# Performance work log

Measured on AMD Instinct MI355X. Metric: run time of the kernel, lower is better.

The kernel has to match this reference:

```python
import jax, jax.numpy as jnp
import numpy as np
from jax import lax

USER_NUM = 60000
ITEM_NUM = 40000
N_NODES = USER_NUM + ITEM_NUM
EMB = 64
NNZ = 3200000
N_LAYERS = 3
ALPHA = 0.1


def setup_inputs() -> dict:
    key = jax.random.key(0)
    k1, k2, k3, k4, k5 = jax.random.split(key, 5)
    rows = jax.random.randint(k1, (NNZ,), 0, N_NODES, dtype=jnp.int32)
    cols = jax.random.randint(k2, (NNZ,), 0, N_NODES, dtype=jnp.int32)
    # normalized adjacency values are small positives
    vals = jax.random.uniform(k3, (NNZ,), dtype=jnp.float32) * 0.05
    user_emb = jax.random.normal(k4, (USER_NUM, EMB), dtype=jnp.float32) * 0.1
    item_emb = jax.random.normal(k5, (ITEM_NUM, EMB), dtype=jnp.float32) * 0.1
    return {"rows": rows, "cols": cols, "vals": vals,
            "user_emb": user_emb, "item_emb": item_emb}


def reference(rows, cols, vals, user_emb, item_emb):
    # ego = cat(user, item); e_out starts at zeros (first forward call).
    ego = jnp.concatenate([user_emb, item_emb], axis=0)  # [N, d]
    e0 = jnp.zeros_like(ego)

    def step(e, _):
        # torch.sparse.mm(A, e.clone().detach()) -> SpMM with stop_gradient,
        # matching the original's detach of the propagated state.
        gathered = vals[:, None] * lax.stop_gradient(e)[cols]  # [nnz, d]
        msg = jax.ops.segment_sum(gathered, rows, num_segments=N_NODES)
        e_new = (1.0 - ALPHA) * msg + ego
        return e_new, None

    e_out, _ = lax.scan(step, e0, None, length=N_LAYERS)
    return e_out[:USER_NUM], e_out[USER_NUM:]
```

## Files before the change

kernel.cpp:

```cpp
#include <hip/hip_runtime.h>
#include <hip/hip_fp16.h>


#define USER_NUM 60000
#define ITEM_NUM 40000
#define N_NODES  100000
#define EMB      64
#define NNZ      3200000
#define OMA       0.9f
#define BR       128
#define NB       782
#define TILE     4096
#define CAPB     4480
#define EPT      9

typedef float f32x4 __attribute__((ext_vector_type(4)));

__global__ __launch_bounds__(512) void bucket_scatter(const int* __restrict__ rows,
                                                      const int* __restrict__ cols,
                                                      const float* __restrict__ vals,
                                                      const float* __restrict__ ue,
                                                      const float* __restrict__ ie,
                                                      __half* __restrict__ ego_h,
                                                      int* __restrict__ bcursor,
                                                      int2* __restrict__ ebuf) {
    __shared__ int bins[NB + 1];
    __shared__ int lcur[NB];
    __shared__ int wsum[8];
    __shared__ int2 stage[TILE];
    __shared__ unsigned short sbk[TILE];
    int t = threadIdx.x;
    int lane = t & 63, w = t >> 6;

    {
        const int total8 = N_NODES * EMB / 8;
        const size_t usz = (size_t)USER_NUM * EMB;
        int u0 = blockIdx.x * 1024;
#pragma unroll
        for (int q = 0; q < 2; ++q) {
            int u = u0 + t + 512 * q;
            if (u < total8) {
                size_t f0 = (size_t)u * 8;
                const float4* s4 = (f0 < usz) ? (const float4*)(ue + f0)
                                              : (const float4*)(ie + (f0 - usz));
                float4 x = s4[0], y = s4[1];
                union { float4 f4; __half2 h2[4]; } o;
                o.h2[0] = __floats2half2_rn(x.x, x.y);
                o.h2[1] = __floats2half2_rn(x.z, x.w);
                o.h2[2] = __floats2half2_rn(y.x, y.y);
                o.h2[3] = __floats2half2_rn(y.z, y.w);
                ((float4*)ego_h)[u] = o.f4;
            }
        }
    }

    for (int b = t; b <= NB; b += 512) bins[b] = 0;
    __syncthreads();

    int e0 = blockIdx.x * TILE;
    int mybk[8], mypk[8];
    float myv[8];
#pragma unroll
    for (int j = 0; j < 8; ++j) {
        int i = e0 + t + 512 * j;
        mybk[j] = -1;
        if (i < NNZ) {
            int r = rows[i], c = cols[i];
            myv[j]  = vals[i] * OMA;
            mybk[j] = r >> 7;
            mypk[j] = c | ((r & 127) << 17);
            atomicAdd(&bins[mybk[j]], 1);
        }
    }
    __syncthreads();

    int b0 = t * 2;
    int r0 = (b0     < NB) ? bins[b0]     : 0;
    int r1 = (b0 + 1 < NB) ? bins[b0 + 1] : 0;
    int s = r0 + r1;
    int incl = s;
#pragma unroll
    for (int off = 1; off < 64; off <<= 1) {
        int v = __shfl_up(incl, off, 64);
        if (lane >= off) incl += v;
    }
    if (lane == 63) wsum[w] = incl;
    __syncthreads();
    int prefix = 0;
#pragma unroll
    for (int i = 0; i < 8; ++i) if (i < w) prefix += wsum[i];
    int excl = prefix + incl - s;
    if (b0     < NB) { bins[b0]     = excl; lcur[b0]     = excl; excl += r0; }
    if (b0 + 1 < NB) { bins[b0 + 1] = excl; lcur[b0 + 1] = excl; }
    if (t == 511) bins[NB] = prefix + incl;
    __syncthreads();

#pragma unroll
    for (int j = 0; j < 8; ++j) {
        if (mybk[j] >= 0) {
            int p = atomicAdd(&lcur[mybk[j]], 1);
            stage[p] = make_int2(mypk[j], __float_as_int(myv[j]));
            sbk[p] = (unsigned short)mybk[j];
        }
    }
    __syncthreads();

    for (int b = t; b < NB; b += 512) {
        int st = bins[b], en = bins[b + 1];
        int c = en - st;
        if (c > 0) lcur[b] = b * CAPB + atomicAdd(&bcursor[b], c) - st;
    }
    __syncthreads();

    int total = bins[NB];
    for (int i = t; i < total; i += 512) {
        int bk = sbk[i];
        ebuf[(size_t)(lcur[bk] + i)] = stage[i];
    }
}

__global__ __launch_bounds__(512) void sort_spmm1(const int* __restrict__ bcursor,
                                                  int2* __restrict__ ebuf,
                                                  int* __restrict__ row_start,
                                                  int* __restrict__ row_end,
                                                  const __half* __restrict__ ego_h,
                                                  const float* __restrict__ ue,
                                                  const float* __restrict__ ie,
                                                  __half* __restrict__ e2h) {
    __shared__ int2 stage[CAPB];
    __shared__ int rhist[BR], rofs[BR], rcur[BR];
    int bk = blockIdx.x, t = threadIdx.x;
    int s = bk * CAPB;
    int cnt = min(bcursor[bk], CAPB);

    if (t < BR) rhist[t] = 0;
    __syncthreads();

    int2 ev[EPT]; int erow[EPT];
#pragma unroll
    for (int j = 0; j < EPT; ++j) {
        int i = t + 512 * j;
        erow[j] = -1;
        if (i < cnt) {
            ev[j] = ebuf[(size_t)(s + i)];
            erow[j] = (ev[j].x >> 17) & 127;
            atomicAdd(&rhist[erow[j]], 1);
        }
    }
    __syncthreads();
    if (t < 64) {
        int h0 = rhist[2 * t], h1 = rhist[2 * t + 1];
        int pair = h0 + h1;
        int incl = pair;
#pragma unroll
        for (int off = 1; off < 64; off <<= 1) {
            int v = __shfl_up(incl, off, 64);
            if (t >= off) incl += v;
        }
        int base = incl - pair;
        rofs[2 * t]     = base;      rcur[2 * t]     = base;
        rofs[2 * t + 1] = base + h0; rcur[2 * t + 1] = base + h0;
    }
    __syncthreads();
    if (t < BR) {
        int r = (bk << 7) + t;
        if (r < N_NODES) {
            row_start[r] = s + rofs[t];
            row_end[r]   = s + rofs[t] + rhist[t];
        }
    }
#pragma unroll
    for (int j = 0; j < EPT; ++j) {
        if (erow[j] >= 0) {
            int p = atomicAdd(&rcur[erow[j]], 1);
            stage[p] = ev[j];
        }
    }
    __syncthreads();
    for (int i = t; i < cnt; i += 512) ebuf[(size_t)(s + i)] = stage[i];

    int lane  = t & 15;
    int qbase = (t & 63) & ~15;
    int g = t >> 4;
    const float2* srcv = (const float2*)ego_h;
#pragma unroll
    for (int rr = 0; rr < 4; ++rr) {
        int rl = (g << 2) | rr;
        int r  = (bk << 7) + rl;
        if (r >= N_NODES) break;
        const float* egop = (r < USER_NUM) ? (ue + (size_t)r * EMB)
                                           : (ie + (size_t)(r - USER_NUM) * EMB);
        float4 acc = ((const float4*)egop)[lane];
        int ss = rofs[rl];
        int ee = ss + rhist[rl];
        for (int k = ss; k < ee; k += 16) {
            int idx = k + lane;
            int2 cv = (idx < ee) ? stage[idx] : make_int2(0, 0);
#pragma unroll
            for (int j = 0; j < 16; ++j) {
                int   cj = __shfl(cv.x, qbase + j, 64) & 0x1FFFF;
                float vj = __int_as_float(__shfl(cv.y, qbase + j, 64));
                union { float2 f2; __half2 h2[2]; } u;
                u.f2 = srcv[(size_t)cj * 16 + lane];
                float2 a = __half22float2(u.h2[0]);
                float2 b = __half22float2(u.h2[1]);
                acc.x += vj * a.x; acc.y += vj * a.y;
                acc.z += vj * b.x; acc.w += vj * b.y;
            }
        }
        union { float2 f2; __half2 h2[2]; } o;
        o.h2[0] = __floats2half2_rn(acc.x, acc.y);
        o.h2[1] = __floats2half2_rn(acc.z, acc.w);
        ((float2*)e2h)[(size_t)r * 16 + lane] = o.f2;
    }
}

__global__ __launch_bounds__(256) void spmm2(const int* __restrict__ row_start,
                                             const int* __restrict__ row_end,
                                             const int2* __restrict__ colval,
                                             const __half* __restrict__ src,
                                             const float* __restrict__ ue,
                                             const float* __restrict__ ie,
                                             float* __restrict__ outb) {
    int tid = blockIdx.x * 256 + threadIdx.x;
    int r = tid >> 4;
    if (r >= N_NODES) return;
    int lane  = threadIdx.x & 15;
    int qbase = (threadIdx.x & 63) & ~15;

    const float* egop = (r < USER_NUM) ? (ue + (size_t)r * EMB)
                                       : (ie + (size_t)(r - USER_NUM) * EMB);
    float4 acc = ((const float4*)egop)[lane];
    const float2* srcv = (const float2*)src;
    const unsigned long long* cv8 = (const unsigned long long*)colval;
    int s = row_start[r], e = row_end[r];

    unsigned long long cv = 0;
    if (s + lane < e) cv = __builtin_nontemporal_load(&cv8[(size_t)(s + lane)]);
    for (int k = s; k < e; k += 16) {
        int idxn = k + 16 + lane;
        unsigned long long nv = 0;
        if (idxn < e) nv = __builtin_nontemporal_load(&cv8[(size_t)idxn]);
        int cx = (int)(cv & 0xFFFFFFFFull), cy = (int)(cv >> 32);
#pragma unroll
        for (int j = 0; j < 16; ++j) {
            int   cj = __shfl(cx, qbase + j, 64) & 0x1FFFF;
            float vj = __int_as_float(__shfl(cy, qbase + j, 64));
            union { float2 f2; __half2 h2[2]; } u;
            u.f2 = srcv[(size_t)cj * 16 + lane];
            float2 a = __half22float2(u.h2[0]);
            float2 b = __half22float2(u.h2[1]);
            acc.x += vj * a.x; acc.y += vj * a.y;
            acc.z += vj * b.x; acc.w += vj * b.y;
        }
        cv = nv;
    }
    f32x4 av = { acc.x, acc.y, acc.z, acc.w };
    __builtin_nontemporal_store(av, &((f32x4*)outb)[(size_t)r * 16 + lane]);
}

extern "C" void kernel_launch(void* const* d_in, const int* in_sizes, int n_in,
                              void* d_out, int out_size, void* d_ws, size_t ws_size,
                              hipStream_t stream) {
    const int*   rows = (const int*)d_in[0];
    const int*   cols = (const int*)d_in[1];
    const float* vals = (const float*)d_in[2];
    const float* ue   = (const float*)d_in[3];
    const float* ie   = (const float*)d_in[4];
    float* out = (float*)d_out;

    char* ws = (char*)d_ws;
    __half* ego_h    = (__half*)ws;
    __half* e2h      = (__half*)(ws + 12800000);
    int2*   ebuf     = (int2*)(ws + 25600000);
    int*    row_s    = (int*)(ws + 53626880);
    int*    row_e    = (int*)(ws + 54026880);
    int*    bcursor  = (int*)(ws + 54426880);

    hipMemsetAsync(bcursor, 0, NB * sizeof(int), stream);

    const int tiles = (NNZ + TILE - 1) / TILE;
    bucket_scatter<<<tiles, 512, 0, stream>>>(rows, cols, vals, ue, ie, ego_h,
                                              bcursor, ebuf);
    sort_spmm1<<<NB, 512, 0, stream>>>(bcursor, ebuf, row_s, row_e, ego_h, ue, ie, e2h);

    const int spmmBlocks = (N_NODES * 16 + 255) / 256;
    spmm2<<<spmmBlocks, 256, 0, stream>>>(row_s, row_e, ebuf, e2h, ue, ie, out);
}
```

Before: 264.3 us.

## Restructure final SpMM to per-bucket blocks staging edges in LDS

The last SpMM pass now runs one 512-thread block per row bucket, matching sort_spmm1, instead of one 16-lane group per row. Each block bulk-loads its sorted edge bucket into shared memory before the row loops. The ego term is read from the half-precision ego buffer instead of the fp32 user/item arrays, and the input edge arrays in bucket_scatter are read with nontemporal loads. This replaces scattered per-row global edge reads with one coalesced bucket load and halves the ego read traffic. In exchange, fp16 rounding of the ego term enters the result, and 782 blocks each serialize 4 rows per group, which risks load imbalance and lower occupancy from the large LDS stage.

Measured after the change: 268.8 us. Within noise of the previous version (+1.7%).

```diff
diff --git a/kernel.cpp b/kernel.cpp
--- a/kernel.cpp
+++ b/kernel.cpp
@@ -65,8 +65,9 @@
         int i = e0 + t + 512 * j;
         mybk[j] = -1;
         if (i < NNZ) {
-            int r = rows[i], c = cols[i];
-            myv[j]  = vals[i] * OMA;
+            int r = __builtin_nontemporal_load(&rows[i]);
+            int c = __builtin_nontemporal_load(&cols[i]);
+            myv[j]  = __builtin_nontemporal_load(&vals[i]) * OMA;
             mybk[j] = r >> 7;
             mypk[j] = c | ((r & 127) << 17);
             atomicAdd(&bins[mybk[j]], 1);
@@ -124,8 +125,6 @@
                                                   int* __restrict__ row_start,
                                                   int* __restrict__ row_end,
                                                   const __half* __restrict__ ego_h,
-                                                  const float* __restrict__ ue,
-                                                  const float* __restrict__ ie,
                                                   __half* __restrict__ e2h) {
     __shared__ int2 stage[CAPB];
     __shared__ int rhist[BR], rofs[BR], rcur[BR];
@@ -188,9 +187,11 @@
         int rl = (g << 2) | rr;
         int r  = (bk << 7) + rl;
         if (r >= N_NODES) break;
-        const float* egop = (r < USER_NUM) ? (ue + (size_t)r * EMB)
-                                           : (ie + (size_t)(r - USER_NUM) * EMB);
-        float4 acc = ((const float4*)egop)[lane];
+        union { float2 f2; __half2 h2[2]; } ei;
+        ei.f2 = srcv[(size_t)r * 16 + lane];
+        float2 i0 = __half22float2(ei.h2[0]);
+        float2 i1 = __half22float2(ei.h2[1]);
+        float4 acc = make_float4(i0.x, i0.y, i1.x, i1.y);
         int ss = rofs[rl];
         int ee = ss + rhist[rl];
         for (int k = ss; k < ee; k += 16) {
@@ -215,48 +216,59 @@
     }
 }
 
-__global__ __launch_bounds__(256) void spmm2(const int* __restrict__ row_start,
+__global__ __launch_bounds__(512) void spmm2(const int* __restrict__ bcursor,
+                                             const int* __restrict__ row_start,
                                              const int* __restrict__ row_end,
-                                             const int2* __restrict__ colval,
+                                             const int2* __restrict__ ebuf,
                                              const __half* __restrict__ src,
-                                             const float* __restrict__ ue,
-                                             const float* __restrict__ ie,
+                                             const __half* __restrict__ ego_h,
                                              float* __restrict__ outb) {
-    int tid = blockIdx.x * 256 + threadIdx.x;
-    int r = tid >> 4;
-    if (r >= N_NODES) return;
-    int lane  = threadIdx.x & 15;
-    int qbase = (threadIdx.x & 63) & ~15;
-
-    const float* egop = (r < USER_NUM) ? (ue + (size_t)r * EMB)
-                                       : (ie + (size_t)(r - USER_NUM) * EMB);
-    float4 acc = ((const float4*)egop)[lane];
+    __shared__ int2 stage[CAPB];
+    int bk = blockIdx.x, t = threadIdx.x;
+    int s = bk * CAPB;
+    int cnt = min(bcursor[bk], CAPB);
+
+    const unsigned long long* eb8 = (const unsigned long long*)ebuf;
+    unsigned long long* st8 = (unsigned long long*)stage;
+    for (int i = t; i < cnt; i += 512)
+        st8[i] = __builtin_nontemporal_load(&eb8[(size_t)(s + i)]);
+    __syncthreads();
+
+    int lane  = t & 15;
+    int qbase = (t & 63) & ~15;
+    int g = t >> 4;
     const float2* srcv = (const float2*)src;
-    const unsigned long long* cv8 = (const unsigned long long*)colval;
-    int s = row_start[r], e = row_end[r];
-
-    unsigned long long cv = 0;
-    if (s + lane < e) cv = __builtin_nontemporal_load(&cv8[(size_t)(s + lane)]);
-    for (int k = s; k < e; k += 16) {
-        int idxn = k + 16 + lane;
-        unsigned long long nv = 0;
-        if (idxn < e) nv = __builtin_nontemporal_load(&cv8[(size_t)idxn]);
-        int cx = (int)(cv & 0xFFFFFFFFull), cy = (int)(cv >> 32);
-#pragma unroll
-        for (int j = 0; j < 16; ++j) {
-            int   cj = __shfl(cx, qbase + j, 64) & 0x1FFFF;
-            float vj = __int_as_float(__shfl(cy, qbase + j, 64));
-            union { float2 f2; __half2 h2[2]; } u;
-            u.f2 = srcv[(size_t)cj * 16 + lane];
-            float2 a = __half22float2(u.h2[0]);
-            float2 b = __half22float2(u.h2[1]);
-            acc.x += vj * a.x; acc.y += vj * a.y;
-            acc.z += vj * b.x; acc.w += vj * b.y;
-        }
-        cv = nv;
-    }
-    f32x4 av = { acc.x, acc.y, acc.z, acc.w };
-    __builtin_nontemporal_store(av, &((f32x4*)outb)[(size_t)r * 16 + lane]);
+    const float2* egov = (const float2*)ego_h;
+#pragma unroll
+    for (int rr = 0; rr < 4; ++rr) {
+        int rl = (g << 2) | rr;
+        int r  = (bk << 7) + rl;
+        if (r >= N_NODES) break;
+        union { float2 f2; __half2 h2[2]; } ei;
+        ei.f2 = egov[(size_t)r * 16 + lane];
+        float2 i0 = __half22float2(ei.h2[0]);
+        float2 i1 = __half22float2(ei.h2[1]);
+        float4 acc = make_float4(i0.x, i0.y, i1.x, i1.y);
+        int ss = row_start[r] - s;
+        int ee = row_end[r] - s;
+        for (int k = ss; k < ee; k += 16) {
+            int idx = k + lane;
+            int2 cv = (idx < ee) ? stage[idx] : make_int2(0, 0);
+#pragma unroll
+            for (int j = 0; j < 16; ++j) {
+                int   cj = __shfl(cv.x, qbase + j, 64) & 0x1FFFF;
+                float vj = __int_as_float(__shfl(cv.y, qbase + j, 64));
+                union { float2 f2; __half2 h2[2]; } u;
+                u.f2 = srcv[(size_t)cj * 16 + lane];
+                float2 a = __half22float2(u.h2[0]);
+                float2 b = __half22float2(u.h2[1]);
+                acc.x += vj * a.x; acc.y += vj * a.y;
+                acc.z += vj * b.x; acc.w += vj * b.y;
+            }
+        }
+        f32x4 av = { acc.x, acc.y, acc.z, acc.w };
+        __builtin_nontemporal_store(av, &((f32x4*)outb)[(size_t)r * 16 + lane]);
+    }
 }
 
 extern "C" void kernel_launch(void* const* d_in, const int* in_sizes, int n_in,
@@ -282,8 +294,6 @@
     const int tiles = (NNZ + TILE - 1) / TILE;
     bucket_scatter<<<tiles, 512, 0, stream>>>(rows, cols, vals, ue, ie, ego_h,
                                               bcursor, ebuf);
-    sort_spmm1<<<NB, 512, 0, stream>>>(bcursor, ebuf, row_s, row_e, ego_h, ue, ie, e2h);
-
-    const int spmmBlocks = (N_NODES * 16 + 255) / 256;
-    spmm2<<<spmmBlocks, 256, 0, stream>>>(row_s, row_e, ebuf, e2h, ue, ie, out);
-}
+    sort_spmm1<<<NB, 512, 0, stream>>>(bcursor, ebuf, row_s, row_e, ego_h, e2h);
+    spmm2<<<NB, 512, 0, stream>>>(bcursor, row_s, row_e, ebuf, e2h, ego_h, out);
+}
```
